# Performance work log

Measured on AMD Instinct MI355X. Metric: run time of the kernel, lower is better.

## Reference

```python
import jax, jax.numpy as jnp
import numpy as np

B, S, D, L = 2, 1024, 1024, 8
HQ, HK, DH = 16, 4, 64          # query heads, kv heads, head_dim = D // HQ
FF, V = 2816, 32000             # FFN hidden (2/3*4D rounded to 256), vocab
EPS = 1e-5
THETA = 500000.0


def setup_inputs() -> dict:
    key = jax.random.key(0)
    ks = jax.random.split(key, 12)
    s = 0.02
    n = lambda k, sh: jax.random.normal(k, sh, dtype=jnp.float32) * s
    return {
        "tokens": jax.random.randint(ks[0], (B, S), 0, V),
        "start_pos": 0,
        "tok_emb": n(ks[1], (V, D)),
        "wq": n(ks[2], (L, D, HQ * DH)),
        "wk": n(ks[3], (L, D, HK * DH)),
        "wv": n(ks[4], (L, D, HK * DH)),
        "wo": n(ks[5], (L, HQ * DH, D)),
        "w1": n(ks[6], (L, D, FF)),
        "w2": n(ks[7], (L, FF, D)),
        "w3": n(ks[8], (L, D, FF)),
        "attn_norm_w": jnp.ones((L, D), jnp.float32),
        "ffn_norm_w": jnp.ones((L, D), jnp.float32),
        "final_norm_w": jnp.ones((D,), jnp.float32),
        "out_w": n(ks[9], (D, V)),
    }


def _rope_cos_sin(start, seqlen):
    freqs = 1.0 / (THETA ** (jnp.arange(0, DH, 2, dtype=jnp.float32) / DH))  # [DH/2]
    t = jnp.arange(start, start + seqlen, dtype=jnp.float32)
    ang = jnp.outer(t, freqs)  # [S, DH/2]
    return jnp.cos(ang), jnp.sin(ang)


def _apply_rope(x, cos, sin):
    # x: [B,S,H,DH]; pairs (even, odd) rotated by complex freqs_cis, as in apply_rotary_emb
    xr = x.reshape(x.shape[:-1] + (DH // 2, 2))
    a, b = xr[..., 0], xr[..., 1]
    c = cos[None, :, None, :]
    s = sin[None, :, None, :]
    out = jnp.stack([a * c - b * s, a * s + b * c], axis=-1)
    return out.reshape(x.shape)


def _rmsnorm(x, w):
    return x * jax.lax.rsqrt(jnp.mean(x * x, axis=-1, keepdims=True) + EPS) * w


def reference(tokens, start_pos, tok_emb, wq, wk, wv, wo, w1, w2, w3,
              attn_norm_w, ffn_norm_w, final_norm_w, out_w):
    h = tok_emb[tokens]  # [B,S,D]
    cos, sin = _rope_cos_sin(start_pos, S)
    # strictly-upper-triangular -inf causal mask (seqlen > 1 branch)
    idx = jnp.arange(S)
    mask = jnp.where(idx[None, :] > idx[:, None], -jnp.inf, 0.0).astype(h.dtype)

    def block(h, p):
        wq_, wk_, wv_, wo_, w1_, w2_, w3_, anw, fnw = p
        x = _rmsnorm(h, anw)
        q = (x @ wq_).reshape(B, S, HQ, DH)
        k = (x @ wk_).reshape(B, S, HK, DH)
        v = (x @ wv_).reshape(B, S, HK, DH)
        q = _apply_rope(q, cos, sin)
        k = _apply_rope(k, cos, sin)
        # start_pos=0: cache slice [:, :seqlen] == freshly written k/v; GQA repeat_kv
        k = jnp.repeat(k, HQ // HK, axis=2)  # [B,S,HQ,DH]
        v = jnp.repeat(v, HQ // HK, axis=2)
        scores = jnp.einsum('bqhd,bkhd->bhqk', q, k) / (DH ** 0.5) + mask
        attn = jax.nn.softmax(scores.astype(jnp.float32), axis=-1).astype(q.dtype)
        o = jnp.einsum('bhqk,bkhd->bqhd', attn, v).reshape(B, S, HQ * DH)
        h = h + o @ wo_
        x2 = _rmsnorm(h, fnw)
        ff = (jax.nn.silu(x2 @ w1_) * (x2 @ w3_)) @ w2_
        return h + ff, None

    h, _ = jax.lax.scan(block, h, (wq, wk, wv, wo, w1, w2, w3, attn_norm_w, ffn_norm_w))
    return (_rmsnorm(h, final_norm_w) @ out_w).astype(jnp.float32)
```

## Files before the change

kernel.cpp:

```cpp
#include <hip/hip_runtime.h>
#include <hip/hip_bf16.h>

typedef __bf16 bf16;
typedef __bf16 bf16x8 __attribute__((ext_vector_type(8)));
typedef float f32x4 __attribute__((ext_vector_type(4)));

#define B_ 2
#define S_ 1024
#define D_ 1024
#define L_ 8
#define HQ_ 16
#define HK_ 4
#define DH_ 64
#define FF_ 2816
#define V_ 32000

#define LGKM0 { asm volatile("s_waitcnt lgkmcnt(0)" ::: "memory"); __builtin_amdgcn_sched_barrier(0); }

__global__ __launch_bounds__(256) void embed_k(const int* __restrict__ toks,
                                               const float* __restrict__ emb,
                                               float* __restrict__ h) {
  int row = blockIdx.x;
  int tok = toks[row];
  f32x4 v = *(const f32x4*)&emb[(size_t)tok * D_ + threadIdx.x * 4];
  *(f32x4*)&h[(size_t)row * D_ + threadIdx.x * 4] = v;
}

__global__ __launch_bounds__(256) void ropetab_k(float* __restrict__ tab) {
  int i = blockIdx.x * 256 + threadIdx.x;
  if (i >= S_ * 32) return;
  int d = i & 31, s = i >> 5;
  float f = expf(-(2.0f * d / 64.0f) * logf(500000.0f));
  float ang = (float)s * f;
  tab[i * 2]     = cosf(ang);
  tab[i * 2 + 1] = sinf(ang);
}

__global__ __launch_bounds__(256) void rmsnorm_k(const float* __restrict__ x,
                                                 const float* __restrict__ w,
                                                 bf16* __restrict__ out) {
  int row = blockIdx.x;
  const float* xr = x + (size_t)row * D_;
  int base = threadIdx.x * 4;
  f32x4 v = *(const f32x4*)&xr[base];
  float ss = v[0]*v[0] + v[1]*v[1] + v[2]*v[2] + v[3]*v[3];
  for (int m = 1; m < 64; m <<= 1) ss += __shfl_xor(ss, m, 64);
  __shared__ float partial[4];
  if ((threadIdx.x & 63) == 0) partial[threadIdx.x >> 6] = ss;
  __syncthreads();
  float tot = partial[0] + partial[1] + partial[2] + partial[3];
  float rr = rsqrtf(tot * (1.0f / D_) + 1e-5f);
  f32x4 wv = *(const f32x4*)&w[base];
  bf16* o = out + (size_t)row * D_ + base;
  o[0] = (bf16)(v[0] * rr * wv[0]);
  o[1] = (bf16)(v[1] * rr * wv[1]);
  o[2] = (bf16)(v[2] * rr * wv[2]);
  o[3] = (bf16)(v[3] * rr * wv[3]);
}

__global__ __launch_bounds__(256) void redrms_k(const float* __restrict__ p,
                                                float* __restrict__ h,
                                                const float* __restrict__ w,
                                                bf16* __restrict__ out) {
  int row = blockIdx.x;
  int base = threadIdx.x * 4;
  size_t ix = (size_t)row * D_ + base;
  f32x4 a = *(const f32x4*)&p[ix];
  f32x4 bb = *(const f32x4*)&p[ix + 2097152];
  f32x4 v = *(const f32x4*)&h[ix];
  v += a + bb;
  *(f32x4*)&h[ix] = v;
  float ss = v[0]*v[0] + v[1]*v[1] + v[2]*v[2] + v[3]*v[3];
  for (int m = 1; m < 64; m <<= 1) ss += __shfl_xor(ss, m, 64);
  __shared__ float partial[4];
  if ((threadIdx.x & 63) == 0) partial[threadIdx.x >> 6] = ss;
  __syncthreads();
  float tot = partial[0] + partial[1] + partial[2] + partial[3];
  float rr = rsqrtf(tot * (1.0f / D_) + 1e-5f);
  f32x4 wv = *(const f32x4*)&w[base];
  bf16* o = out + (size_t)row * D_ + base;
  o[0] = (bf16)(v[0] * rr * wv[0]);
  o[1] = (bf16)(v[1] * rr * wv[1]);
  o[2] = (bf16)(v[2] * rr * wv[2]);
  o[3] = (bf16)(v[3] * rr * wv[3]);
}

__global__ __launch_bounds__(256) void transpose_cvt(const float* __restrict__ src,
                                                     bf16* __restrict__ dst,
                                                     int K, int N,
                                                     long long srcStride, long long dstStride,
                                                     int rowMul, int rowAdd) {
  __shared__ float tile[32][33];
  int bx = blockIdx.x, by = blockIdx.y, z = blockIdx.z;
  src += (size_t)z * srcStride;
  dst += (size_t)z * dstStride;
  int tx = threadIdx.x & 31, ty = threadIdx.x >> 5;
#pragma unroll
  for (int i = 0; i < 4; ++i) {
    int r = ty + i * 8;
    tile[r][tx] = src[(size_t)(by * 32 + r) * N + bx * 32 + tx];
  }
  __syncthreads();
#pragma unroll
  for (int i = 0; i < 4; ++i) {
    int r = ty + i * 8;
    dst[(size_t)((bx * 32 + r) * rowMul + rowAdd) * K + by * 32 + tx] = (bf16)tile[tx][r];
  }
}

template <int EPI, int BM>
__global__ __launch_bounds__(256) void gemm_bt(const bf16* __restrict__ A,
                                               const bf16* __restrict__ BT,
                                               void* __restrict__ Cout,
                                               const float* __restrict__ R,
                                               int M, int N, int K,
                                               int lda, int ldb,
                                               int zKoff, long long partStride) {
  constexpr int MR = BM / 32;
  __shared__ bf16 As[BM * 64];
  __shared__ bf16 Bs[128 * 64];
  const int t = threadIdx.x;
  const int w = t >> 6, l = t & 63;
  const int l15 = l & 15, l4 = l >> 4;
  const int bm = blockIdx.x * BM, bn = blockIdx.y * 128;
  const int wr = w >> 1, wc = w & 1;
  const int z = blockIdx.z;

  const bf16* Az = A + (size_t)z * zKoff;
  const bf16* Bz = BT + (size_t)z * zKoff;
  float* Cz = (float*)Cout + (size_t)z * partStride;

  const int srow = t >> 3, scol = (t & 7) * 8;
  const bf16* ag = &Az[(size_t)(bm + srow) * lda + scol];
  const bf16* bg = &Bz[(size_t)(bn + srow) * ldb + scol];
  const int ldsbase = (t & 192) * 8;

  f32x4 acc[MR][4] = {};

  for (int k0 = 0; k0 < K; k0 += 64) {
#pragma unroll
    for (int i = 0; i < BM / 32; ++i)
      __builtin_amdgcn_global_load_lds(
          (const __attribute__((address_space(1))) void*)(ag + (size_t)(i * 32) * lda + k0),
          (__attribute__((address_space(3))) void*)&As[i * 2048 + ldsbase], 16, 0, 0);
#pragma unroll
    for (int i = 0; i < 4; ++i)
      __builtin_amdgcn_global_load_lds(
          (const __attribute__((address_space(1))) void*)(bg + (size_t)(i * 32) * ldb + k0),
          (__attribute__((address_space(3))) void*)&Bs[i * 2048 + ldsbase], 16, 0, 0);
    __syncthreads();
#pragma unroll
    for (int kc = 0; kc < 2; ++kc) {
      bf16x8 af[MR], bfr[4];
#pragma unroll
      for (int m = 0; m < MR; ++m)
        af[m] = *(const bf16x8*)&As[(wr * (BM / 2) + m * 16 + l15) * 64 + kc * 32 + l4 * 8];
#pragma unroll
      for (int n = 0; n < 4; ++n)
        bfr[n] = *(const bf16x8*)&Bs[(wc * 64 + n * 16 + l15) * 64 + kc * 32 + l4 * 8];
#pragma unroll
      for (int m = 0; m < MR; ++m)
#pragma unroll
        for (int n = 0; n < 4; ++n)
          acc[m][n] = __builtin_amdgcn_mfma_f32_16x16x32_bf16(af[m], bfr[n], acc[m][n], 0, 0, 0);
    }
    __syncthreads();
  }

#pragma unroll
  for (int m = 0; m < MR; ++m)
#pragma unroll
    for (int n = 0; n < 4; ++n)
#pragma unroll
      for (int r = 0; r < 4; ++r) {
        int row = bm + wr * (BM / 2) + m * 16 + l4 * 4 + r;
        int col = bn + wc * 64 + n * 16 + l15;
        size_t ix = (size_t)row * N + col;
        float v = acc[m][n][r];
        if (EPI == 0)      Cz[ix] = v;
        else               Cz[ix] = v + R[ix];
      }
}

template <int EPI>
__global__ __launch_bounds__(512, 2) void gemm256_bt(const bf16* __restrict__ A,
                                                     const bf16* __restrict__ BT,
                                                     void* __restrict__ Cout,
                                                     const float* __restrict__ R,
                                                     int N, int K) {
  extern __shared__ char smem[];
  const int t = threadIdx.x;
  const int wid = t >> 6, l = t & 63;
  const int l15 = l & 15, l4 = l >> 4;
  const int wr = wid >> 2, wc = wid & 3;
  const int rsw = (l4 ^ ((l15 >> 1) & 3)) * 16;
  const int csw = ((t & 3) ^ ((t >> 3) & 3)) * 8;

  int nwg = gridDim.x;
  int q = nwg >> 3, r = nwg & 7;
  int xcd = blockIdx.x & 7, jj = blockIdx.x >> 3;
  int L = (xcd < r ? xcd * (q + 1) : r * (q + 1) + (xcd - r) * q) + jj;
  const int bm = (L & 7) * 256, bn = (L >> 3) * 256;

  const int NT = K >> 6;

  auto stage = [&](const bf16* __restrict__ G, int rowbase, int cbase, int buf, int kc, int kt) {
#pragma unroll
    for (int i = 0; i < 2; ++i) {
      int j = i * 512 + t;
      const bf16* src = G + (size_t)(rowbase + (j >> 2)) * K + kt * 64 + kc * 32 + csw;
      __builtin_amdgcn_global_load_lds(
          (const __attribute__((address_space(1))) void*)src,
          (__attribute__((address_space(3))) void*)(smem + cbase + buf * 32768 + kc * 16384 +
                                                    i * 8192 + wid * 1024),
          16, 0, 0);
    }
  };
  auto ldA = [&](int buf, int kc, int m) -> bf16x8 {
    return *(const bf16x8*)(smem + buf * 32768 + kc * 16384 +
                            (wr * 128 + m * 16 + l15) * 64 + rsw);
  };
  auto ldB = [&](int buf, int kc, int n) -> bf16x8 {
    return *(const bf16x8*)(smem + 65536 + buf * 32768 + kc * 16384 +
                            (wc * 64 + n * 16 + l15) * 64 + rsw);
  };

  f32x4 acc[8][4] = {};
  bf16x8 af[4], bq[4];

  auto rd03 = [&](int buf, int kc) {
#pragma unroll
    for (int m = 0; m < 4; ++m) af[m] = ldA(buf, kc, m);
#pragma unroll
    for (int n = 0; n < 4; ++n) bq[n] = ldB(buf, kc, n);
  };
  auto rd47 = [&](int buf, int kc) {
#pragma unroll
    for (int m = 0; m < 4; ++m) af[m] = ldA(buf, kc, 4 + m);
  };
  auto mf_lo = [&]() {
    __builtin_amdgcn_s_setprio(1);
#pragma unroll
    for (int m = 0; m < 4; ++m)
#pragma unroll
      for (int n = 0; n < 4; ++n)
        acc[m][n] = __builtin_amdgcn_mfma_f32_16x16x32_bf16(af[m], bq[n], acc[m][n], 0, 0, 0);
    __builtin_amdgcn_s_setprio(0);
    __builtin_amdgcn_sched_barrier(0);
  };
  auto mf_hi = [&]() {
    __builtin_amdgcn_s_setprio(1);
#pragma unroll
    for (int m = 0; m < 4; ++m)
#pragma unroll
      for (int n = 0; n < 4; ++n)
        acc[4 + m][n] = __builtin_amdgcn_mfma_f32_16x16x32_bf16(af[m], bq[n], acc[4 + m][n], 0, 0, 0);
    __builtin_amdgcn_s_setprio(0);
    __builtin_amdgcn_sched_barrier(0);
  };
#define GBAR { __builtin_amdgcn_sched_barrier(0); __builtin_amdgcn_s_barrier(); }
#define VMW(n) { asm volatile("s_waitcnt vmcnt(" #n ")" ::: "memory"); __builtin_amdgcn_sched_barrier(0); }

  stage(A, bm, 0, 0, 0, 0);  stage(BT, bn, 65536, 0, 0, 0);
  stage(A, bm, 0, 0, 1, 0);  stage(BT, bn, 65536, 0, 1, 0);
  stage(A, bm, 0, 1, 0, 1);  stage(BT, bn, 65536, 1, 0, 1);
  VMW(8);
  __builtin_amdgcn_s_barrier();

  for (int kt = 0; kt < NT - 2; ++kt) {
    const int buf = kt & 1, nbuf = buf ^ 1;
    rd03(buf, 0);
    stage(A, bm, 0, nbuf, 1, kt + 1);
    GBAR; mf_lo(); GBAR;
    rd47(buf, 0);
    stage(BT, bn, 65536, nbuf, 1, kt + 1);
    GBAR; mf_hi(); VMW(8); __builtin_amdgcn_s_barrier();
    rd03(buf, 1);
    stage(A, bm, 0, buf, 0, kt + 2);
    stage(BT, bn, 65536, buf, 0, kt + 2);
    GBAR; mf_lo(); GBAR;
    rd47(buf, 1);
    GBAR; mf_hi(); VMW(8); __builtin_amdgcn_s_barrier();
  }
  {
    const int kt = NT - 2;
    const int buf = kt & 1, nbuf = buf ^ 1;
    rd03(buf, 0);
    stage(A, bm, 0, nbuf, 1, kt + 1);
    GBAR; mf_lo(); GBAR;
    rd47(buf, 0);
    stage(BT, bn, 65536, nbuf, 1, kt + 1);
    GBAR; mf_hi(); VMW(8); __builtin_amdgcn_s_barrier();
    rd03(buf, 1);
    GBAR; mf_lo(); GBAR;
    rd47(buf, 1);
    GBAR; mf_hi(); VMW(4); __builtin_amdgcn_s_barrier();
  }
  {
    const int buf = (NT - 1) & 1;
    rd03(buf, 0);
    GBAR; mf_lo(); GBAR;
    rd47(buf, 0);
    GBAR; mf_hi(); VMW(0); __builtin_amdgcn_s_barrier();
    rd03(buf, 1);
    GBAR; mf_lo(); GBAR;
    rd47(buf, 1);
    GBAR; mf_hi(); __builtin_amdgcn_s_barrier();
  }
#undef GBAR
#undef VMW

#pragma unroll
  for (int m = 0; m < 8; ++m)
#pragma unroll
    for (int n = 0; n < 4; ++n)
#pragma unroll
      for (int rr = 0; rr < 4; ++rr) {
        int row = bm + wr * 128 + m * 16 + l4 * 4 + rr;
        int col = bn + wc * 64 + n * 16 + l15;
        size_t ix = (size_t)row * N + col;
        float v = acc[m][n][rr];
        if (EPI == 0)      ((float*)Cout)[ix] = v;
        else if (EPI == 1) ((float*)Cout)[ix] = v + R[ix];
        else               ((bf16*)Cout)[ix] = (bf16)v;
      }
}

template <int EPI>
__global__ __launch_bounds__(512, 4) void gemm8_bt(const bf16* __restrict__ A,
                                                   const bf16* __restrict__ BT,
                                                   void* __restrict__ Cout,
                                                   const float* __restrict__ tab,
                                                   bf16* __restrict__ krout,
                                                   bf16* __restrict__ vtout,
                                                   int N, int K) {
  extern __shared__ char smem[];
  const int t = threadIdx.x;
  const int wid = t >> 6, l = t & 63;
  const int l15 = l & 15, l4 = l >> 4;
  const int wr = wid >> 1, wc = wid & 1;
  const int rsw = (l4 ^ ((l15 >> 1) & 3)) * 16;
  const int csw = ((t & 3) ^ ((t >> 3) & 3)) * 8;

  int nwg = gridDim.x;
  int q = nwg >> 3;
  int xcd = blockIdx.x & 7, jj = blockIdx.x >> 3;
  int L = xcd * q + jj;
  const int bm = (L & 15) * 128, bn = (L >> 4) * 128;

  const int NT = K >> 6;

  auto stage = [&](const bf16* __restrict__ G, int rowbase, int obase, int buf, int kc, int kt) {
    const bf16* src = G + (size_t)(rowbase + (t >> 2)) * K + kt * 64 + kc * 32 + csw;
    __builtin_amdgcn_global_load_lds(
        (const __attribute__((address_space(1))) void*)src,
        (__attribute__((address_space(3))) void*)(smem + obase + buf * 16384 + kc * 8192 +
                                                  wid * 1024),
        16, 0, 0);
  };
  auto ldA = [&](int buf, int kc, int m) -> bf16x8 {
    return *(const bf16x8*)(smem + buf * 16384 + kc * 8192 +
                            (wr * 32 + m * 16 + l15) * 64 + rsw);
  };
  auto ldB = [&](int buf, int kc, int n) -> bf16x8 {
    return *(const bf16x8*)(smem + 32768 + buf * 16384 + kc * 8192 +
                            (wc * 64 + n * 16 + l15) * 64 + rsw);
  };

  f32x4 acc[2][4] = {};
  bf16x8 af[2], bq[4];

  auto rdph = [&](int buf, int kc) {
#pragma unroll
    for (int m = 0; m < 2; ++m) af[m] = ldA(buf, kc, m);
#pragma unroll
    for (int n = 0; n < 4; ++n) bq[n] = ldB(buf, kc, n);
  };
  auto mf = [&]() {
    __builtin_amdgcn_s_setprio(1);
#pragma unroll
    for (int m = 0; m < 2; ++m)
#pragma unroll
      for (int n = 0; n < 4; ++n)
        acc[m][n] = __builtin_amdgcn_mfma_f32_16x16x32_bf16(af[m], bq[n], acc[m][n], 0, 0, 0);
    __builtin_amdgcn_s_setprio(0);
    __builtin_amdgcn_sched_barrier(0);
  };
#define SCB __builtin_amdgcn_sched_barrier(0)
#define VMW4 { asm volatile("s_waitcnt vmcnt(4)" ::: "memory"); SCB; }
#define VMW2 { asm volatile("s_waitcnt vmcnt(2)" ::: "memory"); SCB; }
#define VMW0 { asm volatile("s_waitcnt vmcnt(0)" ::: "memory"); SCB; }
#define SBAR { __builtin_amdgcn_s_barrier(); SCB; }

  stage(A, bm, 0, 0, 0, 0);  stage(BT, bn, 32768, 0, 0, 0);
  stage(A, bm, 0, 0, 1, 0);  stage(BT, bn, 32768, 0, 1, 0);
  stage(A, bm, 0, 1, 0, 1);  stage(BT, bn, 32768, 1, 0, 1);
  VMW4; __builtin_amdgcn_s_barrier();

  for (int kt = 0; kt < NT - 2; ++kt) {
    const int buf = kt & 1, nbuf = buf ^ 1;
    rdph(buf, 0);
    stage(A, bm, 0, nbuf, 1, kt + 1);
    stage(BT, bn, 32768, nbuf, 1, kt + 1);
    SCB; mf(); VMW4; SBAR;
    rdph(buf, 1);
    stage(A, bm, 0, buf, 0, kt + 2);
    stage(BT, bn, 32768, buf, 0, kt + 2);
    SCB; mf(); VMW4; SBAR;
  }
  {
    const int buf = (NT - 2) & 1, nbuf = buf ^ 1;
    rdph(buf, 0);
    stage(A, bm, 0, nbuf, 1, NT - 1);
    stage(BT, bn, 32768, nbuf, 1, NT - 1);
    SCB; mf(); VMW4; SBAR;
    rdph(buf, 1);
    SCB; mf(); VMW2; SBAR;
  }
  {
    const int buf = (NT - 1) & 1;
    rdph(buf, 0);
    SCB; mf(); VMW0; SBAR;
    rdph(buf, 1);
    SCB; mf();
  }
#undef SCB
#undef VMW4
#undef VMW2
#undef VMW0
#undef SBAR

  __builtin_amdgcn_s_barrier();

  if (EPI == 3) {
    bf16* wb = (bf16*)(smem + wid * 2304);
    bf16* G = (bf16*)Cout;
    const int Nc = N >> 1;
#pragma unroll
    for (int m = 0; m < 2; ++m) {
#pragma unroll
      for (int n = 0; n < 4; ++n)
#pragma unroll
        for (int rr = 0; rr < 4; ++rr) {
          float v = acc[m][n][rr];
          float part = __shfl_xor(v, 1, 64);
          if (!(l15 & 1)) {
            float s = v / (1.0f + __expf(-v));
            wb[(l4 * 4 + rr) * 40 + n * 8 + (l15 >> 1)] = (bf16)(s * part);
          }
        }
      LGKM0;
      int ROW = l >> 2, CB = l & 3;
      bf16x8 g = *(const bf16x8*)&wb[ROW * 40 + CB * 8];
      LGKM0;
      int row = bm + wr * 32 + m * 16 + ROW;
      int col = (bn >> 1) + wc * 32 + CB * 8;
      *(bf16x8*)&G[(size_t)row * Nc + col] = g;
    }
  } else {
    const int cb = bn >> 7;
    if (cb >= 10) {
      bf16* wbT = (bf16*)(smem + wid * 4352);
#pragma unroll
      for (int m = 0; m < 2; ++m)
#pragma unroll
        for (int n = 0; n < 4; ++n)
#pragma unroll
          for (int rr = 0; rr < 4; ++rr)
            wbT[(n * 16 + l15) * 34 + m * 16 + l4 * 4 + rr] = (bf16)acc[m][n][rr];
      LGKM0;
      bf16x8 v0 = *(const bf16x8*)&wbT[l * 34];
      bf16x8 v1 = *(const bf16x8*)&wbT[l * 34 + 8];
      bf16x8 v2 = *(const bf16x8*)&wbT[l * 34 + 16];
      bf16x8 v3 = *(const bf16x8*)&wbT[l * 34 + 24];
      LGKM0;
      int hh = ((bn - 1280) >> 6) + wc;
      int b = bm >> 10;
      int scol = (bm & 1023) + wr * 32;
      bf16* dst = &vtout[((size_t)((b * HK_ + hh) * 64 + l)) * S_ + scol];
      *(bf16x8*)&dst[0]  = v0;  *(bf16x8*)&dst[8]  = v1;
      *(bf16x8*)&dst[16] = v2;  *(bf16x8*)&dst[24] = v3;
    } else {
      bf16* wb = (bf16*)(smem + wid * 2304);
#pragma unroll
      for (int m = 0; m < 2; ++m) {
#pragma unroll
        for (int n = 0; n < 4; ++n)
#pragma unroll
          for (int rr = 0; rr < 4; ++rr)
            wb[(l4 * 4 + rr) * 72 + n * 16 + l15] = (bf16)acc[m][n][rr];
        LGKM0;
        int ROW = l >> 2, CB = l & 3;
        bf16x8 g0 = *(const bf16x8*)&wb[ROW * 72 + CB * 16];
        bf16x8 g1 = *(const bf16x8*)&wb[ROW * 72 + CB * 16 + 8];
        LGKM0;
        int row = bm + wr * 32 + m * 16 + ROW;
        if (cb < 8) {
          bf16* Cb = (bf16*)Cout;
          int col = bn + wc * 64 + CB * 16;
          *(bf16x8*)&Cb[(size_t)row * N + col] = g0;
          *(bf16x8*)&Cb[(size_t)row * N + col + 8] = g1;
        } else {
          int b = row >> 10, ss = row & 1023;
          int hh = ((bn - 1024) >> 6) + wc;
          int d0 = CB * 16;
          f32x4 t0 = *(const f32x4*)&tab[(ss * 32 + (d0 >> 1)) * 2];
          f32x4 t1 = *(const f32x4*)&tab[(ss * 32 + (d0 >> 1)) * 2 + 4];
          f32x4 t2 = *(const f32x4*)&tab[(ss * 32 + (d0 >> 1) + 4) * 2];
          f32x4 t3 = *(const f32x4*)&tab[(ss * 32 + (d0 >> 1) + 4) * 2 + 4];
          bf16x8 r0, r1;
#pragma unroll
          for (int j = 0; j < 4; ++j) {
            float a = (float)g0[2 * j], bv = (float)g0[2 * j + 1];
            float c  = (j < 2 ? t0 : t1)[(j & 1) * 2];
            float sn = (j < 2 ? t0 : t1)[(j & 1) * 2 + 1];
            r0[2 * j]     = (bf16)(a * c - bv * sn);
            r0[2 * j + 1] = (bf16)(a * sn + bv * c);
            float a2 = (float)g1[2 * j], bv2 = (float)g1[2 * j + 1];
            float c2  = (j < 2 ? t2 : t3)[(j & 1) * 2];
            float sn2 = (j < 2 ? t2 : t3)[(j & 1) * 2 + 1];
            r1[2 * j]     = (bf16)(a2 * c2 - bv2 * sn2);
            r1[2 * j + 1] = (bf16)(a2 * sn2 + bv2 * c2);
          }
          bf16* dst = &krout[((size_t)((b * HK_ + hh) * S_ + ss)) * 64 + d0];
          *(bf16x8*)&dst[0] = r0;
          *(bf16x8*)&dst[8] = r1;
        }
      }
    }
  }
}

__global__ __launch_bounds__(256) void attn_k(const bf16* __restrict__ qkv,
                                              const float* __restrict__ tab,
                                              const bf16* __restrict__ k_r,
                                              const bf16* __restrict__ vT,
                                              bf16* __restrict__ o) {
  __shared__ bf16 k_lds[128 * 64];
  __shared__ bf16 v_lds[64 * 128];
  __shared__ bf16 p_lds[4][16 * 136];
  int t = threadIdx.x, w = t >> 6, l = t & 63, l15 = l & 15, l4 = l >> 4;
  int bx = blockIdx.x;
  int qt = bx & 15;
  if (bx >= 256) qt = 15 - qt;
  int head = (bx >> 4) & 15, b = bx >> 8;
  int kvh = head >> 2;
  const bf16* kh = k_r + ((size_t)(b * HK_ + kvh)) * S_ * 64;
  const bf16* vh = vT + ((size_t)(b * HK_ + kvh)) * 64 * S_;
  int q0 = qt * 64 + w * 16;
  const int ntile = (qt + 2) >> 1;

  bf16x8 aq[2];
  {
    int s = q0 + l15;
#pragma unroll
    for (int kc = 0; kc < 2; ++kc) {
      bf16x8 raw = *(const bf16x8*)&qkv[(size_t)(b * S_ + s) * 1536 + head * 64 +
                                        kc * 32 + l4 * 8];
      int d0 = kc * 16 + l4 * 4;
      f32x4 tc0 = *(const f32x4*)&tab[(s * 32 + d0) * 2];
      f32x4 tc1 = *(const f32x4*)&tab[(s * 32 + d0) * 2 + 4];
      bf16x8 out;
#pragma unroll
      for (int j = 0; j < 4; ++j) {
        float a = (float)raw[2 * j], bb = (float)raw[2 * j + 1];
        float c  = (j < 2 ? tc0 : tc1)[(j & 1) * 2];
        float sn = (j < 2 ? tc0 : tc1)[(j & 1) * 2 + 1];
        out[2 * j]     = (bf16)((a * c - bb * sn) * 0.125f);
        out[2 * j + 1] = (bf16)((a * sn + bb * c) * 0.125f);
      }
      aq[kc] = out;
    }
  }

  f32x4 acc_o[4] = {};
  float m_run[4], l_run[4];
#pragma unroll
  for (int r = 0; r < 4; ++r) { m_run[r] = -1e30f; l_run[r] = 0.f; }

  bf16x8 gk[4], gv[4];
#pragma unroll
  for (int i = 0; i < 4; ++i) {
    int c = i * 256 + t;
    gk[i] = *(const bf16x8*)&kh[(size_t)(c >> 3) * 64 + (c & 7) * 8];
    gv[i] = *(const bf16x8*)&vh[(size_t)(c >> 4) * S_ + (c & 15) * 8];
  }

  for (int j = 0; j < ntile; ++j) {
#pragma unroll
    for (int i = 0; i < 4; ++i) {
      int c = i * 256 + t;
      int krow = c >> 3, kch = (c & 7) ^ (krow & 7);
      *(bf16x8*)&k_lds[krow * 64 + kch * 8] = gk[i];
      int vrow = c >> 4, vch = (c & 15) ^ (vrow & 15);
      *(bf16x8*)&v_lds[vrow * 128 + vch * 8] = gv[i];
    }
    __syncthreads();

    bf16x8 gkn[4], gvn[4];
    if (j + 1 < ntile) {
#pragma unroll
      for (int i = 0; i < 4; ++i) {
        int c = i * 256 + t;
        gkn[i] = *(const bf16x8*)&kh[(size_t)((j + 1) * 128 + (c >> 3)) * 64 + (c & 7) * 8];
        gvn[i] = *(const bf16x8*)&vh[(size_t)(c >> 4) * S_ + (j + 1) * 128 + (c & 15) * 8];
      }
    }

    f32x4 sc[8];
#pragma unroll
    for (int nt = 0; nt < 8; ++nt) {
      f32x4 a = {};
#pragma unroll
      for (int kc = 0; kc < 2; ++kc) {
        bf16x8 bk = *(const bf16x8*)&k_lds[(nt * 16 + l15) * 64 +
                                           (((kc * 4 + l4) ^ (l15 & 7)) * 8)];
        a = __builtin_amdgcn_mfma_f32_16x16x32_bf16(aq[kc], bk, a, 0, 0, 0);
      }
      sc[nt] = a;
    }

    bool lastt = (j == ntile - 1);
#pragma unroll
    for (int r = 0; r < 4; ++r) {
      float pmax = -1e30f;
#pragma unroll
      for (int nt = 0; nt < 8; ++nt) {
        float s = sc[nt][r];
        if (lastt) {
          int kj = j * 128 + nt * 16 + l15;
          int qi = q0 + l4 * 4 + r;
          if (kj > qi) s = -1e30f;
        }
        sc[nt][r] = s;
        pmax = fmaxf(pmax, s);
      }
      if (!__all(pmax <= m_run[r] + 8.0f)) {
        float mx = pmax;
        mx = fmaxf(mx, __shfl_xor(mx, 1, 64));
        mx = fmaxf(mx, __shfl_xor(mx, 2, 64));
        mx = fmaxf(mx, __shfl_xor(mx, 4, 64));
        mx = fmaxf(mx, __shfl_xor(mx, 8, 64));
        float mn = fmaxf(m_run[r], mx);
        float scale = __expf(m_run[r] - mn);
        m_run[r] = mn;
        l_run[r] *= scale;
#pragma unroll
        for (int nt = 0; nt < 4; ++nt) acc_o[nt][r] *= scale;
      }
      float rs = 0.f;
#pragma unroll
      for (int nt = 0; nt < 8; ++nt) {
        float p = __expf(sc[nt][r] - m_run[r]);
        sc[nt][r] = p;
        rs += p;
      }
      rs += __shfl_xor(rs, 1, 64);
      rs += __shfl_xor(rs, 2, 64);
      rs += __shfl_xor(rs, 4, 64);
      rs += __shfl_xor(rs, 8, 64);
      l_run[r] += rs;
    }

#pragma unroll
    for (int nt = 0; nt < 8; ++nt)
#pragma unroll
      for (int r = 0; r < 4; ++r)
        p_lds[w][(l4 * 4 + r) * 136 + nt * 16 + l15] = (bf16)sc[nt][r];
    LGKM0;

#pragma unroll
    for (int kc = 0; kc < 4; ++kc) {
      bf16x8 pf = *(const bf16x8*)&p_lds[w][l15 * 136 + kc * 32 + l4 * 8];
#pragma unroll
      for (int nt = 0; nt < 4; ++nt) {
        bf16x8 vf = *(const bf16x8*)&v_lds[(nt * 16 + l15) * 128 +
                                           (((kc * 4 + l4) ^ l15) * 8)];
        acc_o[nt] = __builtin_amdgcn_mfma_f32_16x16x32_bf16(pf, vf, acc_o[nt], 0, 0, 0);
      }
    }
    __syncthreads();

#pragma unroll
    for (int i = 0; i < 4; ++i) { gk[i] = gkn[i]; gv[i] = gvn[i]; }
  }

#pragma unroll
  for (int nt = 0; nt < 4; ++nt)
#pragma unroll
    for (int r = 0; r < 4; ++r) {
      float ov = acc_o[nt][r] / l_run[r];
      int s = qt * 64 + w * 16 + l4 * 4 + r;
      o[((size_t)(b * S_ + s)) * D_ + head * 64 + nt * 16 + l15] = (bf16)ov;
    }
}

extern "C" void kernel_launch(void* const* d_in, const int* in_sizes, int n_in,
                              void* d_out, int out_size, void* d_ws, size_t ws_size,
                              hipStream_t stream) {
  const int* tokens  = (const int*)d_in[0];
  const float* tok_emb = (const float*)d_in[2];
  const float* wq = (const float*)d_in[3];
  const float* wk = (const float*)d_in[4];
  const float* wv = (const float*)d_in[5];
  const float* wo = (const float*)d_in[6];
  const float* w1 = (const float*)d_in[7];
  const float* w2 = (const float*)d_in[8];
  const float* w3 = (const float*)d_in[9];
  const float* anw = (const float*)d_in[10];
  const float* fnw = (const float*)d_in[11];
  const float* finw = (const float*)d_in[12];
  const float* outw = (const float*)d_in[13];

  (void)hipFuncSetAttribute((const void*)gemm256_bt<0>,
                            hipFuncAttributeMaxDynamicSharedMemorySize, 131072);
  (void)hipFuncSetAttribute((const void*)gemm8_bt<3>,
                            hipFuncAttributeMaxDynamicSharedMemorySize, 65536);
  (void)hipFuncSetAttribute((const void*)gemm8_bt<4>,
                            hipFuncAttributeMaxDynamicSharedMemorySize, 65536);

  auto al = [](size_t x) { return (x + 255) & ~(size_t)255; };
  const size_t WTB   = 11272192ull * 2;
  const size_t OUTWTB = (size_t)V_ * D_ * 2;
  const size_t HB   = (size_t)B_ * S_ * D_ * 4;
  const size_t XBB  = (size_t)B_ * S_ * D_ * 2;
  const size_t QKVB = (size_t)B_ * S_ * 1536 * 2;
  const size_t KRB  = (size_t)B_ * HK_ * S_ * 64 * 2;
  const size_t OB   = (size_t)B_ * S_ * D_ * 2;
  const size_t GATEB = (size_t)B_ * S_ * 2816 * 2;
  const size_t TABB = (size_t)S_ * 32 * 2 * 4;
  const size_t PARTB = (size_t)B_ * S_ * D_ * 4 * 2;

  size_t fixed = al(OUTWTB) + al(HB) + al(XBB) + al(QKVB) + al(KRB) + al(KRB) +
                 al(OB) + al(GATEB) + al(TABB) + al(PARTB);
  bool allup = ws_size >= fixed + 8 * al(WTB) + 4096;
  int nslots = allup ? 8 : 1;

  char* p = (char*)d_ws;
  bf16* wT    = (bf16*)p; p += (size_t)nslots * al(WTB);
  bf16* outwT = (bf16*)p; p += al(OUTWTB);
  float* h    = (float*)p; p += al(HB);
  bf16* xb    = (bf16*)p; p += al(XBB);
  bf16* qkv   = (bf16*)p; p += al(QKVB);
  bf16* k_r   = (bf16*)p; p += al(KRB);
  bf16* vTb   = (bf16*)p; p += al(KRB);
  bf16* ob    = (bf16*)p; p += al(OB);
  bf16* gate  = (bf16*)p; p += al(GATEB);
  float* tab  = (float*)p; p += al(TABB);
  float* part = (float*)p; p += al(PARTB);

  const size_t WTS = al(WTB) / 2;
  const size_t OFF_QKV = 0;
  const size_t OFF_WK  = 1024ull * 1024;
  const size_t OFF_WV  = 1280ull * 1024;
  const size_t OFF_WO  = 1572864ull;
  const size_t OFF_W13 = 2621440ull;
  const size_t OFF_W2  = 8388608ull;

  auto tr = [&](const float* src, size_t srcStride, bf16* dst, size_t dstStride,
                int Kd, int Nd, int layers, int rowMul, int rowAdd) {
    transpose_cvt<<<dim3(Nd / 32, Kd / 32, layers), 256, 0, stream>>>(
        src, dst, Kd, Nd, (long long)srcStride, (long long)dstStride, rowMul, rowAdd);
  };

  ropetab_k<<<128, 256, 0, stream>>>(tab);
  embed_k<<<B_ * S_, 256, 0, stream>>>(tokens, tok_emb, h);
  tr(outw, 0, outwT, 0, 1024, 32000, 1, 1, 0);

  if (allup) {
    tr(wq, 1024 * 1024, wT + OFF_QKV, WTS, 1024, 1024, 8, 1, 0);
    tr(wk, 1024 * 256,  wT + OFF_WK,  WTS, 1024, 256, 8, 1, 0);
    tr(wv, 1024 * 256,  wT + OFF_WV,  WTS, 1024, 256, 8, 1, 0);
    tr(wo, 1024 * 1024, wT + OFF_WO,  WTS, 1024, 1024, 8, 1, 0);
    tr(w1, 1024 * 2816, wT + OFF_W13, WTS, 1024, 2816, 8, 2, 0);
    tr(w3, 1024 * 2816, wT + OFF_W13, WTS, 1024, 2816, 8, 2, 1);
    tr(w2, 2816 * 1024, wT + OFF_W2,  WTS, 2816, 1024, 8, 1, 0);
  }

  rmsnorm_k<<<B_ * S_, 256, 0, stream>>>(h, anw, xb);

  for (int l = 0; l < L_; ++l) {
    bf16* wtl = wT + (allup ? (size_t)l * WTS : 0);
    if (!allup) {
      tr(wq + (size_t)l * 1024 * 1024, 0, wtl + OFF_QKV, 0, 1024, 1024, 1, 1, 0);
      tr(wk + (size_t)l * 1024 * 256,  0, wtl + OFF_WK,  0, 1024, 256, 1, 1, 0);
      tr(wv + (size_t)l * 1024 * 256,  0, wtl + OFF_WV,  0, 1024, 256, 1, 1, 0);
      tr(wo + (size_t)l * 1024 * 1024, 0, wtl + OFF_WO,  0, 1024, 1024, 1, 1, 0);
      tr(w1 + (size_t)l * 1024 * 2816, 0, wtl + OFF_W13, 0, 1024, 2816, 1, 2, 0);
      tr(w3 + (size_t)l * 1024 * 2816, 0, wtl + OFF_W13, 0, 1024, 2816, 1, 2, 1);
      tr(w2 + (size_t)l * 2816 * 1024, 0, wtl + OFF_W2,  0, 2816, 1024, 1, 1, 0);
    }

    gemm8_bt<4><<<192, 512, 65536, stream>>>(xb, wtl + OFF_QKV, qkv, tab, k_r, vTb,
                                             1536, 1024);
    attn_k<<<B_ * HQ_ * (S_ / 64), 256, 0, stream>>>(qkv, tab, k_r, vTb, ob);
    gemm_bt<1, 32><<<dim3(64, 8, 1), 256, 0, stream>>>(ob, wtl + OFF_WO, h, h,
                                                       2048, 1024, 1024, 1024, 1024, 0, 0);
    rmsnorm_k<<<B_ * S_, 256, 0, stream>>>(h, fnw + l * D_, xb);
    gemm8_bt<3><<<704, 512, 65536, stream>>>(xb, wtl + OFF_W13, gate, nullptr, nullptr,
                                             nullptr, 5632, 1024);
    gemm_bt<0, 64><<<dim3(32, 8, 2), 256, 0, stream>>>(gate, wtl + OFF_W2, part, nullptr,
                                                       2048, 1024, 1408, 2816, 2816,
                                                       1408, 2097152ll);
    redrms_k<<<B_ * S_, 256, 0, stream>>>(part, h,
                                          (l < L_ - 1) ? (anw + (l + 1) * D_) : finw, xb);
  }

  gemm256_bt<0><<<1000, 512, 131072, stream>>>(xb, outwT, d_out, nullptr, 32000, 1024);
}
```

Measured before the change: 1.467 ms.

## Make LM-head GEMM persistent with next-tile prefetch; defer attention row-sum reduction

The vocab projection GEMM now launches 256 persistent workgroups that loop over the 1000 output tiles. Each workgroup issues the global-to-LDS loads for its next tile before storing the previous tile's accumulators, so epilogue stores overlap with prefetch and the tail-wave imbalance of a 1000-block grid is avoided. Separately, attention no longer shuffle-reduces the softmax row sum on every KV tile. Each lane keeps a partial sum and reduces once before normalisation, which removes cross-lane shuffles from the inner loop. The persistent kernel drops the residual/bf16 epilogue variants and relies on tricky vmcnt accounting across tiles.

```diff
diff --git a/kernel.cpp b/kernel.cpp
--- a/kernel.cpp
+++ b/kernel.cpp
@@ -187,7 +187,7 @@
                                                      const bf16* __restrict__ BT,
                                                      void* __restrict__ Cout,
                                                      const float* __restrict__ R,
-                                                     int N, int K) {
+                                                     int N, int K, int ntiles) {
   extern __shared__ char smem[];
   const int t = threadIdx.x;
   const int wid = t >> 6, l = t & 63;
@@ -196,11 +196,12 @@
   const int rsw = (l4 ^ ((l15 >> 1) & 3)) * 16;
   const int csw = ((t & 3) ^ ((t >> 3) & 3)) * 8;
 
-  int nwg = gridDim.x;
-  int q = nwg >> 3, r = nwg & 7;
-  int xcd = blockIdx.x & 7, jj = blockIdx.x >> 3;
-  int L = (xcd < r ? xcd * (q + 1) : r * (q + 1) + (xcd - r) * q) + jj;
-  const int bm = (L & 7) * 256, bn = (L >> 3) * 256;
+  const int qq = ntiles >> 3, rr8 = ntiles & 7;
+  auto tileLoc = [&](int T, int& obm, int& obn) {
+    int xcd = T & 7, jj = T >> 3;
+    int L = (xcd < rr8 ? xcd * (qq + 1) : rr8 * (qq + 1) + (xcd - rr8) * qq) + jj;
+    obm = (L & 7) * 256; obn = (L >> 3) * 256;
+  };
 
   const int NT = K >> 6;
 
@@ -225,7 +226,7 @@
                             (wc * 64 + n * 16 + l15) * 64 + rsw);
   };
 
-  f32x4 acc[8][4] = {};
+  f32x4 acc[8][4];
   bf16x8 af[4], bq[4];
 
   auto rd03 = [&](int buf, int kc) {
@@ -258,72 +259,93 @@
     __builtin_amdgcn_s_setprio(0);
     __builtin_amdgcn_sched_barrier(0);
   };
+  auto epi_store = [&](int ebm, int ebn) {
+#pragma unroll
+    for (int m = 0; m < 8; ++m)
+#pragma unroll
+      for (int n = 0; n < 4; ++n)
+#pragma unroll
+        for (int rr = 0; rr < 4; ++rr) {
+          int row = ebm + wr * 128 + m * 16 + l4 * 4 + rr;
+          int col = ebn + wc * 64 + n * 16 + l15;
+          ((float*)Cout)[(size_t)row * N + col] = acc[m][n][rr];
+        }
+  };
 #define GBAR { __builtin_amdgcn_sched_barrier(0); __builtin_amdgcn_s_barrier(); }
 #define VMW(n) { asm volatile("s_waitcnt vmcnt(" #n ")" ::: "memory"); __builtin_amdgcn_sched_barrier(0); }
 
+  int bm, bn;
+  tileLoc(blockIdx.x, bm, bn);
   stage(A, bm, 0, 0, 0, 0);  stage(BT, bn, 65536, 0, 0, 0);
   stage(A, bm, 0, 0, 1, 0);  stage(BT, bn, 65536, 0, 1, 0);
   stage(A, bm, 0, 1, 0, 1);  stage(BT, bn, 65536, 1, 0, 1);
-  VMW(8);
-  __builtin_amdgcn_s_barrier();
-
-  for (int kt = 0; kt < NT - 2; ++kt) {
-    const int buf = kt & 1, nbuf = buf ^ 1;
-    rd03(buf, 0);
-    stage(A, bm, 0, nbuf, 1, kt + 1);
-    GBAR; mf_lo(); GBAR;
-    rd47(buf, 0);
-    stage(BT, bn, 65536, nbuf, 1, kt + 1);
-    GBAR; mf_hi(); VMW(8); __builtin_amdgcn_s_barrier();
-    rd03(buf, 1);
-    stage(A, bm, 0, buf, 0, kt + 2);
-    stage(BT, bn, 65536, buf, 0, kt + 2);
-    GBAR; mf_lo(); GBAR;
-    rd47(buf, 1);
-    GBAR; mf_hi(); VMW(8); __builtin_amdgcn_s_barrier();
-  }
-  {
-    const int kt = NT - 2;
-    const int buf = kt & 1, nbuf = buf ^ 1;
-    rd03(buf, 0);
-    stage(A, bm, 0, nbuf, 1, kt + 1);
-    GBAR; mf_lo(); GBAR;
-    rd47(buf, 0);
-    stage(BT, bn, 65536, nbuf, 1, kt + 1);
-    GBAR; mf_hi(); VMW(8); __builtin_amdgcn_s_barrier();
-    rd03(buf, 1);
-    GBAR; mf_lo(); GBAR;
-    rd47(buf, 1);
-    GBAR; mf_hi(); VMW(4); __builtin_amdgcn_s_barrier();
-  }
-  {
-    const int buf = (NT - 1) & 1;
-    rd03(buf, 0);
-    GBAR; mf_lo(); GBAR;
-    rd47(buf, 0);
-    GBAR; mf_hi(); VMW(0); __builtin_amdgcn_s_barrier();
-    rd03(buf, 1);
-    GBAR; mf_lo(); GBAR;
-    rd47(buf, 1);
-    GBAR; mf_hi(); __builtin_amdgcn_s_barrier();
-  }
+
+  bool first = true;
+  int pbm = 0, pbn = 0;
+
+  for (int T = blockIdx.x; T < ntiles; T += 256) {
+    if (!first) epi_store(pbm, pbn);
+#pragma unroll
+    for (int m = 0; m < 8; ++m)
+#pragma unroll
+      for (int n = 0; n < 4; ++n)
+        acc[m][n] = (f32x4){0.f, 0.f, 0.f, 0.f};
+    if (first) { VMW(8); } else { VMW(63); }
+    __builtin_amdgcn_s_barrier();
+
+    for (int kt = 0; kt < NT - 2; ++kt) {
+      const int buf = kt & 1, nbuf = buf ^ 1;
+      rd03(buf, 0);
+      stage(A, bm, 0, nbuf, 1, kt + 1);
+      GBAR; mf_lo(); GBAR;
+      rd47(buf, 0);
+      stage(BT, bn, 65536, nbuf, 1, kt + 1);
+      GBAR; mf_hi(); VMW(8); __builtin_amdgcn_s_barrier();
+      rd03(buf, 1);
+      stage(A, bm, 0, buf, 0, kt + 2);
+      stage(BT, bn, 65536, buf, 0, kt + 2);
+      GBAR; mf_lo(); GBAR;
+      rd47(buf, 1);
+      GBAR; mf_hi(); VMW(8); __builtin_amdgcn_s_barrier();
+    }
+    {
+      const int kt = NT - 2;
+      const int buf = kt & 1, nbuf = buf ^ 1;
+      rd03(buf, 0);
+      stage(A, bm, 0, nbuf, 1, kt + 1);
+      GBAR; mf_lo(); GBAR;
+      rd47(buf, 0);
+      stage(BT, bn, 65536, nbuf, 1, kt + 1);
+      GBAR; mf_hi(); VMW(8); __builtin_amdgcn_s_barrier();
+      rd03(buf, 1);
+      GBAR; mf_lo(); GBAR;
+      rd47(buf, 1);
+      GBAR; mf_hi(); VMW(4); __builtin_amdgcn_s_barrier();
+    }
+    {
+      const int buf = (NT - 1) & 1;
+      rd03(buf, 0);
+      GBAR; mf_lo(); GBAR;
+      rd47(buf, 0);
+      GBAR; mf_hi(); VMW(0); __builtin_amdgcn_s_barrier();
+      rd03(buf, 1);
+      GBAR; mf_lo(); GBAR;
+      rd47(buf, 1);
+      GBAR; mf_hi(); __builtin_amdgcn_s_barrier();
+    }
+
+    pbm = bm; pbn = bn; first = false;
+    int Tn = T + 256;
+    if (Tn < ntiles) {
+      tileLoc(Tn, bm, bn);
+      stage(A, bm, 0, 0, 0, 0);  stage(BT, bn, 65536, 0, 0, 0);
+      stage(A, bm, 0, 0, 1, 0);  stage(BT, bn, 65536, 0, 1, 0);
+      stage(A, bm, 0, 1, 0, 1);  stage(BT, bn, 65536, 1, 0, 1);
+    }
+  }
+  epi_store(pbm, pbn);
 #undef GBAR
 #undef VMW
-
-#pragma unroll
-  for (int m = 0; m < 8; ++m)
-#pragma unroll
-    for (int n = 0; n < 4; ++n)
-#pragma unroll
-      for (int rr = 0; rr < 4; ++rr) {
-        int row = bm + wr * 128 + m * 16 + l4 * 4 + rr;
-        int col = bn + wc * 64 + n * 16 + l15;
-        size_t ix = (size_t)row * N + col;
-        float v = acc[m][n][rr];
-        if (EPI == 0)      ((float*)Cout)[ix] = v;
-        else if (EPI == 1) ((float*)Cout)[ix] = v + R[ix];
-        else               ((bf16*)Cout)[ix] = (bf16)v;
-      }
 }
 
 template <int EPI>
@@ -655,10 +677,6 @@
         sc[nt][r] = p;
         rs += p;
       }
-      rs += __shfl_xor(rs, 1, 64);
-      rs += __shfl_xor(rs, 2, 64);
-      rs += __shfl_xor(rs, 4, 64);
-      rs += __shfl_xor(rs, 8, 64);
       l_run[r] += rs;
     }
 
@@ -683,6 +701,16 @@
 
 #pragma unroll
     for (int i = 0; i < 4; ++i) { gk[i] = gkn[i]; gv[i] = gvn[i]; }
+  }
+
+#pragma unroll
+  for (int r = 0; r < 4; ++r) {
+    float lr = l_run[r];
+    lr += __shfl_xor(lr, 1, 64);
+    lr += __shfl_xor(lr, 2, 64);
+    lr += __shfl_xor(lr, 4, 64);
+    lr += __shfl_xor(lr, 8, 64);
+    l_run[r] = lr;
   }
 
 #pragma unroll
@@ -806,5 +834,5 @@
                                           (l < L_ - 1) ? (anw + (l + 1) * D_) : finw, xb);
   }
 
-  gemm256_bt<0><<<1000, 512, 131072, stream>>>(xb, outwT, d_out, nullptr, 32000, 1024);
-}
+  gemm256_bt<0><<<256, 512, 131072, stream>>>(xb, outwT, d_out, nullptr, 32000, 1024, 1000);
+}
```

Result: no change. 1.448 ms (-1.3%).
